# Kernel optimization log

Measured on AMD Instinct MI355X. Metric: run time of the kernel, lower is better.

## Reference

```python
import jax, jax.numpy as jnp
import numpy as np

N, D, H, C, ED, E = 50000, 128, 8, 16, 16, 800000  # nodes, model dim, heads, head dim, edge dim, edges

def _layer_norm(x, g, b, eps=1e-5):
    mu = x.mean(-1, keepdims=True)
    var = ((x - mu) ** 2).mean(-1, keepdims=True)
    return (x - mu) * jax.lax.rsqrt(var + eps) * g + b

def setup_inputs() -> dict:
    key = jax.random.key(0)
    ks = jax.random.split(key, 24)
    s = 0.05
    inp = {
        'x': jax.random.normal(ks[0], (N, D), jnp.float32),
        'edge_index': jax.random.randint(ks[1], (2, E), 0, N, jnp.int32),
        'edge_attr': jax.random.normal(ks[2], (E, ED), jnp.float32),
        # TransformerConv params (Linear convention: y = x @ W + b)
        'wq': s * jax.random.normal(ks[3], (D, H * C)), 'bq': s * jax.random.normal(ks[4], (H * C,)),
        'wk': s * jax.random.normal(ks[5], (D, H * C)), 'bk': s * jax.random.normal(ks[6], (H * C,)),
        'wv': s * jax.random.normal(ks[7], (D, H * C)), 'bv': s * jax.random.normal(ks[8], (H * C,)),
        'we': s * jax.random.normal(ks[9], (ED, H * C)),            # lin_edge, bias=False
        'wskip': s * jax.random.normal(ks[10], (D, H * C)), 'bskip': s * jax.random.normal(ks[11], (H * C,)),
        'wbeta': s * jax.random.normal(ks[12], (3 * H * C, 1)),     # lin_beta, bias=False
        # norms
        'ln1_g': 1.0 + s * jax.random.normal(ks[13], (D,)), 'ln1_b': s * jax.random.normal(ks[14], (D,)),
        'ln2_g': 1.0 + s * jax.random.normal(ks[15], (D,)), 'ln2_b': s * jax.random.normal(ks[16], (D,)),
        # FFN
        'w1': s * jax.random.normal(ks[17], (D, 2 * D)), 'b1': s * jax.random.normal(ks[18], (2 * D,)),
        'w2': s * jax.random.normal(ks[19], (2 * D, D)), 'b2': s * jax.random.normal(ks[20], (D,)),
    }
    return inp

def reference(x, edge_index, edge_attr, wq, bq, wk, bk, wv, bv, we, wskip, bskip, wbeta,
              ln1_g, ln1_b, ln2_g, ln2_b, w1, b1, w2, b2):
    src, dst = edge_index[0], edge_index[1]  # message flows src (j) -> dst (i)
    # --- pre-norm + TransformerConv (beta=True, concat=True, eval-mode dropout=identity) ---
    xn = _layer_norm(x, ln1_g, ln1_b)
    q = (xn @ wq + bq).reshape(N, H, C)
    k = (xn @ wk + bk).reshape(N, H, C)
    v = (xn @ wv + bv).reshape(N, H, C)
    e = (edge_attr @ we).reshape(E, H, C)
    kj = k[src] + e                                     # [E,H,C]
    alpha = (q[dst] * kj).sum(-1) / jnp.sqrt(jnp.float32(C))  # [E,H]
    # segment softmax over incoming edges per destination node
    m = jax.ops.segment_max(alpha, dst, num_segments=N)        # [N,H]
    ea = jnp.exp(alpha - m[dst])
    denom = jax.ops.segment_sum(ea, dst, num_segments=N)
    alpha = ea / (denom[dst] + 1e-16)
    msg = (v[src] + e) * alpha[..., None]               # [E,H,C]
    out = jax.ops.segment_sum(msg, dst, num_segments=N).reshape(N, H * C)
    # beta-gated skip
    x_r = xn @ wskip + bskip
    beta = jax.nn.sigmoid(jnp.concatenate([out, x_r, out - x_r], axis=-1) @ wbeta)  # [N,1]
    out = beta * x_r + (1.0 - beta) * out
    x = x + out
    # --- pre-norm FFN ---
    h = _layer_norm(x, ln2_g, ln2_b)
    h = jax.nn.gelu(h @ w1 + b1, approximate=False) @ w2 + b2
    return x + h
```

## Files before the change

kernel.cpp:

```cpp
#include <hip/hip_runtime.h>
#include <math.h>

#define N_NODES 50000
#define D_MODEL 128
#define N_HEADS 8
#define HEAD_C 16
#define E_DIM 16
#define N_EDGES 800000

typedef __attribute__((ext_vector_type(8))) short bf16x8;
typedef __attribute__((ext_vector_type(4))) float f32x4;

__device__ inline ushort f2bf(float f) {
    unsigned u = __float_as_uint(f);
    unsigned r = (u + 0x7fffu + ((u >> 16) & 1u)) >> 16;
    return (ushort)r;
}
__device__ inline float bf2f(ushort h) { return __uint_as_float(((unsigned)h) << 16); }
__device__ inline uint pack2(float a, float b) {
    return (uint)f2bf(a) | ((uint)f2bf(b) << 16);
}
__device__ inline float gelu_f(float v) {
    return 0.5f * v * (1.0f + erff(v * 0.70710678118654752f));
}

__global__ void prep_weights(const float* __restrict__ wq, const float* __restrict__ wk,
                             const float* __restrict__ wv, const float* __restrict__ wsk,
                             const float* __restrict__ bq, const float* __restrict__ bk,
                             const float* __restrict__ bv, const float* __restrict__ bsk,
                             const float* __restrict__ w1, const float* __restrict__ w2,
                             ushort* __restrict__ wqkvsT, float* __restrict__ bqkvs,
                             ushort* __restrict__ w1T, ushort* __restrict__ w2T,
                             int* __restrict__ deg)
{
    int idx = blockIdx.x * 256 + threadIdx.x;
    {
        int m = idx >> 7, kk = idx & 127;
        int b = m >> 7, ch = m & 127;
        const float* src = (b == 0) ? wq : (b == 1) ? wk : (b == 2) ? wv : wsk;
        wqkvsT[idx] = f2bf(src[kk * 128 + ch]);
    }
    if (idx < 256 * 128) {
        int m = idx >> 7, k = idx & 127;
        w1T[idx] = f2bf(w1[k * 256 + m]);
    }
    if (idx < 128 * 256) {
        int m = idx >> 8, k = idx & 255;
        w2T[idx] = f2bf(w2[k * 128 + m]);
    }
    if (idx < 512) {
        int b = idx >> 7, ch = idx & 127;
        const float* bb = (b == 0) ? bq : (b == 1) ? bk : (b == 2) ? bv : bsk;
        bqkvs[idx] = bb[ch];
    }
    if (idx < N_NODES) deg[idx] = 0;
}

__global__ __launch_bounds__(256) void proj_ln_gemm(
    const float* __restrict__ X, const float* __restrict__ ln_g, const float* __restrict__ ln_b,
    const ushort* __restrict__ WT, const float* __restrict__ bias,
    ushort* __restrict__ Y, int nrows)
{
    __shared__ __align__(16) ushort Al[128 * 128];
    __shared__ __align__(16) ushort Wl[128 * 128];
    int tid = threadIdx.x;
    int wv = tid >> 6, lane = tid & 63;
    int row0 = blockIdx.x * 128;
    int col0 = blockIdx.y * 128;

    int c16 = tid & 15;
    float4 g0 = *(const float4*)&ln_g[c16 * 8];
    float4 g1 = *(const float4*)&ln_g[c16 * 8 + 4];
    float4 bb0 = *(const float4*)&ln_b[c16 * 8];
    float4 bb1 = *(const float4*)&ln_b[c16 * 8 + 4];

    #pragma unroll
    for (int i = 0; i < 8; ++i) {
        int c = tid + i * 256;
        int r = c >> 4;
        int gr = row0 + r;
        float4 xa = make_float4(0.f, 0.f, 0.f, 0.f), xb = xa;
        if (gr < nrows) {
            xa = *(const float4*)&X[(size_t)gr * 128 + c16 * 8];
            xb = *(const float4*)&X[(size_t)gr * 128 + c16 * 8 + 4];
        }
        float s  = xa.x + xa.y + xa.z + xa.w + xb.x + xb.y + xb.z + xb.w;
        float ss = xa.x*xa.x + xa.y*xa.y + xa.z*xa.z + xa.w*xa.w
                 + xb.x*xb.x + xb.y*xb.y + xb.z*xb.z + xb.w*xb.w;
        #pragma unroll
        for (int m = 1; m < 16; m <<= 1) {
            s  += __shfl_xor(s,  m, 64);
            ss += __shfl_xor(ss, m, 64);
        }
        float mu  = s * (1.0f / 128.0f);
        float var = ss * (1.0f / 128.0f) - mu * mu;
        float rs  = rsqrtf(var + 1e-5f);
        ushort h[8];
        h[0] = f2bf((xa.x - mu) * rs * g0.x + bb0.x);
        h[1] = f2bf((xa.y - mu) * rs * g0.y + bb0.y);
        h[2] = f2bf((xa.z - mu) * rs * g0.z + bb0.z);
        h[3] = f2bf((xa.w - mu) * rs * g0.w + bb0.w);
        h[4] = f2bf((xb.x - mu) * rs * g1.x + bb1.x);
        h[5] = f2bf((xb.y - mu) * rs * g1.y + bb1.y);
        h[6] = f2bf((xb.z - mu) * rs * g1.z + bb1.z);
        h[7] = f2bf((xb.w - mu) * rs * g1.w + bb1.w);
        int byte = r * 256 + ((c16 * 16) ^ ((r & 7) << 4));
        *(ulonglong2*)((char*)Al + byte) = *(ulonglong2*)h;
    }
    #pragma unroll
    for (int i = 0; i < 8; ++i) {
        int c = tid + i * 256;
        int r = c >> 4, cc = c & 15;
        ulonglong2 val = *(const ulonglong2*)(WT + (size_t)(col0 + r) * 128 + cc * 8);
        int byte = r * 256 + ((cc * 16) ^ ((r & 7) << 4));
        *(ulonglong2*)((char*)Wl + byte) = val;
    }
    __syncthreads();

    f32x4 acc[2][8];
    #pragma unroll
    for (int i = 0; i < 2; ++i)
        #pragma unroll
        for (int j = 0; j < 8; ++j) acc[i][j] = (f32x4){0.f, 0.f, 0.f, 0.f};
    #pragma unroll
    for (int ks = 0; ks < 4; ++ks) {
        bf16x8 af[2], bfr[8];
        #pragma unroll
        for (int rt = 0; rt < 2; ++rt) {
            int r = wv * 32 + rt * 16 + (lane & 15);
            int byte = r * 256 + ((ks * 64 + (lane >> 4) * 16) ^ ((r & 7) << 4));
            af[rt] = *(const bf16x8*)((const char*)Al + byte);
        }
        #pragma unroll
        for (int ct = 0; ct < 8; ++ct) {
            int r = ct * 16 + (lane & 15);
            int byte = r * 256 + ((ks * 64 + (lane >> 4) * 16) ^ ((r & 7) << 4));
            bfr[ct] = *(const bf16x8*)((const char*)Wl + byte);
        }
        #pragma unroll
        for (int rt = 0; rt < 2; ++rt)
            #pragma unroll
            for (int ct = 0; ct < 8; ++ct)
                acc[rt][ct] = __builtin_amdgcn_mfma_f32_16x16x32_bf16(
                    af[rt], bfr[ct], acc[rt][ct], 0, 0, 0);
    }
    #pragma unroll
    for (int rt = 0; rt < 2; ++rt) {
        #pragma unroll
        for (int ct = 0; ct < 8; ++ct) {
            int gcol = col0 + ct * 16 + (lane & 15);
            float bv = bias[gcol];
            #pragma unroll
            for (int r = 0; r < 4; ++r) {
                int grow = row0 + wv * 32 + rt * 16 + (lane >> 4) * 4 + r;
                if (grow >= nrows) continue;
                Y[(size_t)grow * 512 + gcol] = f2bf(acc[rt][ct][r] + bv);
            }
        }
    }
}

__global__ __launch_bounds__(256) void ffn_fused(
    const ushort* __restrict__ A, const ushort* __restrict__ W1T,
    const ushort* __restrict__ W2T, const float* __restrict__ b1,
    const float* __restrict__ b2, const float* __restrict__ xnew,
    float* __restrict__ out, int nrows)
{
    __shared__ __align__(16) ushort Xl[128 * 128];
    __shared__ __align__(16) ushort W1l[64 * 128];
    __shared__ __align__(16) ushort Hl[128 * 64];
    __shared__ __align__(16) ushort W2l[128 * 64];
    int tid = threadIdx.x;
    int wv = tid >> 6, lane = tid & 63;
    int row0 = blockIdx.x * 128;

    #pragma unroll
    for (int i = 0; i < 8; ++i) {
        int c = tid + i * 256;
        int r = c >> 4, c16 = c & 15;
        int gr = row0 + r;
        ulonglong2 val = {0ull, 0ull};
        if (gr < nrows) val = *(const ulonglong2*)(A + (size_t)gr * 128 + c16 * 8);
        int byte = r * 256 + ((c16 * 16) ^ ((r & 7) << 4));
        *(ulonglong2*)((char*)Xl + byte) = val;
    }

    f32x4 acc2[2][8];
    #pragma unroll
    for (int i = 0; i < 2; ++i)
        #pragma unroll
        for (int j = 0; j < 8; ++j) acc2[i][j] = (f32x4){0.f, 0.f, 0.f, 0.f};

    for (int q = 0; q < 4; ++q) {
        #pragma unroll
        for (int i = 0; i < 4; ++i) {
            int c = tid + i * 256;
            int r = c >> 4, cc = c & 15;
            ulonglong2 val = *(const ulonglong2*)(W1T + (size_t)(q * 64 + r) * 128 + cc * 8);
            int byte = r * 256 + ((cc * 16) ^ ((r & 7) << 4));
            *(ulonglong2*)((char*)W1l + byte) = val;
        }
        #pragma unroll
        for (int i = 0; i < 4; ++i) {
            int c = tid + i * 256;
            int r = c >> 3, c8 = c & 7;
            ulonglong2 val = *(const ulonglong2*)(W2T + (size_t)r * 256 + q * 64 + c8 * 8);
            int byte = r * 128 + ((c8 * 16) ^ ((r & 7) << 4));
            *(ulonglong2*)((char*)W2l + byte) = val;
        }
        __syncthreads();

        f32x4 acc1[2][4];
        #pragma unroll
        for (int i = 0; i < 2; ++i)
            #pragma unroll
            for (int j = 0; j < 4; ++j) acc1[i][j] = (f32x4){0.f, 0.f, 0.f, 0.f};
        #pragma unroll
        for (int ks = 0; ks < 4; ++ks) {
            bf16x8 af[2], bfr[4];
            #pragma unroll
            for (int rt = 0; rt < 2; ++rt) {
                int r = wv * 32 + rt * 16 + (lane & 15);
                int byte = r * 256 + ((ks * 64 + (lane >> 4) * 16) ^ ((r & 7) << 4));
                af[rt] = *(const bf16x8*)((const char*)Xl + byte);
            }
            #pragma unroll
            for (int ct = 0; ct < 4; ++ct) {
                int r = ct * 16 + (lane & 15);
                int byte = r * 256 + ((ks * 64 + (lane >> 4) * 16) ^ ((r & 7) << 4));
                bfr[ct] = *(const bf16x8*)((const char*)W1l + byte);
            }
            #pragma unroll
            for (int rt = 0; rt < 2; ++rt)
                #pragma unroll
                for (int ct = 0; ct < 4; ++ct)
                    acc1[rt][ct] = __builtin_amdgcn_mfma_f32_16x16x32_bf16(
                        af[rt], bfr[ct], acc1[rt][ct], 0, 0, 0);
        }
        #pragma unroll
        for (int rt = 0; rt < 2; ++rt) {
            #pragma unroll
            for (int ct = 0; ct < 4; ++ct) {
                int cl = ct * 16 + (lane & 15);
                float bv = b1[q * 64 + cl];
                #pragma unroll
                for (int r = 0; r < 4; ++r) {
                    int row = wv * 32 + rt * 16 + (lane >> 4) * 4 + r;
                    float v = gelu_f(acc1[rt][ct][r] + bv);
                    int cb = cl * 2;
                    int byte = row * 128 + ((cb & ~15) ^ ((row & 7) << 4)) + (cb & 15);
                    *(ushort*)((char*)Hl + byte) = f2bf(v);
                }
            }
        }
        __syncthreads();

        #pragma unroll
        for (int ks = 0; ks < 2; ++ks) {
            bf16x8 af[2], bfr[8];
            #pragma unroll
            for (int rt = 0; rt < 2; ++rt) {
                int row = wv * 32 + rt * 16 + (lane & 15);
                int byte = row * 128 + ((ks * 64 + (lane >> 4) * 16) ^ ((row & 7) << 4));
                af[rt] = *(const bf16x8*)((const char*)Hl + byte);
            }
            #pragma unroll
            for (int ct = 0; ct < 8; ++ct) {
                int r = ct * 16 + (lane & 15);
                int byte = r * 128 + ((ks * 64 + (lane >> 4) * 16) ^ ((r & 7) << 4));
                bfr[ct] = *(const bf16x8*)((const char*)W2l + byte);
            }
            #pragma unroll
            for (int rt = 0; rt < 2; ++rt)
                #pragma unroll
                for (int ct = 0; ct < 8; ++ct)
                    acc2[rt][ct] = __builtin_amdgcn_mfma_f32_16x16x32_bf16(
                        af[rt], bfr[ct], acc2[rt][ct], 0, 0, 0);
        }
        __syncthreads();
    }

    #pragma unroll
    for (int rt = 0; rt < 2; ++rt) {
        #pragma unroll
        for (int ct = 0; ct < 8; ++ct) {
            int gcol = ct * 16 + (lane & 15);
            float bv = b2[gcol];
            #pragma unroll
            for (int r = 0; r < 4; ++r) {
                int grow = row0 + wv * 32 + rt * 16 + (lane >> 4) * 4 + r;
                if (grow >= nrows) continue;
                size_t idx = (size_t)grow * 128 + gcol;
                out[idx] = acc2[rt][ct][r] + bv + xnew[idx];
            }
        }
    }
}

__global__ void hist_kernel(const int* __restrict__ dst, int* __restrict__ deg)
{
    int e = blockIdx.x * 256 + threadIdx.x;
    if (e < N_EDGES) atomicAdd(&deg[dst[e]], 1);
}

__global__ void scan1_kernel(const int* __restrict__ deg, int* __restrict__ off,
                             int* __restrict__ bsum)
{
    __shared__ int sm[256];
    int i = blockIdx.x * 256 + threadIdx.x;
    int v = (i < N_NODES) ? deg[i] : 0;
    sm[threadIdx.x] = v;
    __syncthreads();
    #pragma unroll
    for (int d = 1; d < 256; d <<= 1) {
        int t = (threadIdx.x >= d) ? sm[threadIdx.x - d] : 0;
        __syncthreads();
        sm[threadIdx.x] += t;
        __syncthreads();
    }
    if (i < N_NODES) off[i] = sm[threadIdx.x] - v;
    if (threadIdx.x == 255) bsum[blockIdx.x] = sm[255];
}

__global__ void scan2_kernel(int* __restrict__ bsum, int nb)
{
    __shared__ int sm[256];
    int v = (threadIdx.x < nb) ? bsum[threadIdx.x] : 0;
    sm[threadIdx.x] = v;
    __syncthreads();
    #pragma unroll
    for (int d = 1; d < 256; d <<= 1) {
        int t = (threadIdx.x >= d) ? sm[threadIdx.x - d] : 0;
        __syncthreads();
        sm[threadIdx.x] += t;
        __syncthreads();
    }
    if (threadIdx.x < nb) bsum[threadIdx.x] = sm[threadIdx.x] - v;
}

__global__ void scan3_kernel(int* __restrict__ off, const int* __restrict__ bsum,
                             int* __restrict__ cursor)
{
    int i = blockIdx.x * 256 + threadIdx.x;
    if (i < N_NODES) {
        int o = off[i] + bsum[blockIdx.x];
        off[i] = o;
        cursor[i] = o;
    }
}

__global__ void scatter_kernel(const int* __restrict__ dst, const int* __restrict__ src,
                               const float* __restrict__ eattr, int* __restrict__ cursor,
                               int* __restrict__ src_s, ushort* __restrict__ eattr_s)
{
    int e = blockIdx.x * 256 + threadIdx.x;
    if (e < N_EDGES) {
        int p = atomicAdd(&cursor[dst[e]], 1);
        src_s[p] = src[e];
        const float4* s4 = (const float4*)(eattr + (size_t)e * E_DIM);
        float4 f0 = s4[0], f1 = s4[1], f2 = s4[2], f3 = s4[3];
        uint4 u0, u1;
        u0.x = pack2(f0.x, f0.y); u0.y = pack2(f0.z, f0.w);
        u0.z = pack2(f1.x, f1.y); u0.w = pack2(f1.z, f1.w);
        u1.x = pack2(f2.x, f2.y); u1.y = pack2(f2.z, f2.w);
        u1.z = pack2(f3.x, f3.y); u1.w = pack2(f3.z, f3.w);
        uint4* d4 = (uint4*)(eattr_s + (size_t)p * E_DIM);
        d4[0] = u0; d4[1] = u1;
    }
}

#define ATTN_STEP(P, S, A0, A1, E0, E1) do {                                         \
    int sv_ = src_s[P];                                                              \
    uint eap_ = *(const uint*)(eattr_s + (size_t)(P) * E_DIM + j2);                  \
    float ea0_ = bf2f((ushort)eap_), ea1_ = bf2f((ushort)(eap_ >> 16));              \
    size_t sb_ = (size_t)sv_ * 512;                                                  \
    uint kp_ = *(const uint*)(qkvs + sb_ + 128 + 2 * lane);                          \
    uint vp_ = *(const uint*)(qkvs + sb_ + 256 + 2 * lane);                          \
    float p_ = q0 * bf2f((ushort)kp_) + q1 * bf2f((ushort)(kp_ >> 16))               \
             + ea0_ * qp0 + ea1_ * qp1;                                              \
    p_ += __shfl_xor(p_, 1, 64);                                                     \
    p_ += __shfl_xor(p_, 2, 64);                                                     \
    p_ += __shfl_xor(p_, 4, 64);                                                     \
    float w_ = __expf(fminf(p_, 60.f));                                              \
    S  += w_;                                                                        \
    A0 += w_ * bf2f((ushort)vp_);                                                    \
    A1 += w_ * bf2f((ushort)(vp_ >> 16));                                            \
    E0 += w_ * ea0_;                                                                 \
    E1 += w_ * ea1_;                                                                 \
} while (0)

__global__ void node_attn(const ushort* __restrict__ qkvs, const float* __restrict__ x,
                          const float* __restrict__ we, const float* __restrict__ wbeta,
                          const float* __restrict__ ln2g, const float* __restrict__ ln2b,
                          const int* __restrict__ off, const int* __restrict__ deg,
                          const int* __restrict__ src_s, const ushort* __restrict__ eattr_s,
                          float* __restrict__ xnew, ushort* __restrict__ h2)
{
    __shared__ float wl[E_DIM * 128];
    __shared__ float weT[128 * 17];
    __shared__ float sc4[4][128];
    for (int t = threadIdx.x; t < E_DIM * 32; t += 256)
        *(float4*)&wl[t * 4] = *(const float4*)&we[t * 4];
    for (int t = threadIdx.x; t < E_DIM * 128; t += 256) {
        int j = t >> 7, ch = t & 127;
        weT[ch * 17 + j] = we[t];
    }
    __syncthreads();

    int nl   = threadIdx.x >> 6;
    int node = blockIdx.x * 4 + nl;
    int lane = threadIdx.x & 63;
    if (node >= N_NODES) return;

    int j2 = (lane & 7) * 2;
    int hb = (lane >> 3) * 16;

    size_t nb = (size_t)node * 512;
    uint qp = *(const uint*)(qkvs + nb + 2 * lane);
    float q0r = bf2f((ushort)qp), q1r = bf2f((ushort)(qp >> 16));

    sc4[nl][2 * lane]     = q0r;
    sc4[nl][2 * lane + 1] = q1r;
    float qp0 = 0.f, qp1 = 0.f;
    #pragma unroll
    for (int c = 0; c < 16; ++c) {
        float qc = sc4[nl][hb + c];
        qp0 += qc * weT[(hb + c) * 17 + j2];
        qp1 += qc * weT[(hb + c) * 17 + j2 + 1];
    }
    float q0 = q0r * 0.25f, q1 = q1r * 0.25f;
    qp0 *= 0.25f; qp1 *= 0.25f;

    float SA = 0.f, A0a = 0.f, A1a = 0.f, E0a = 0.f, E1a = 0.f;
    float SB = 0.f, A0b = 0.f, A1b = 0.f, E0b = 0.f, E1b = 0.f;

    int o = off[node], dg = deg[node];
    int i = 0;
    for (; i + 2 <= dg; i += 2) {
        ATTN_STEP(o + i,     SA, A0a, A1a, E0a, E1a);
        ATTN_STEP(o + i + 1, SB, A0b, A1b, E0b, E1b);
    }
    if (i < dg)
        ATTN_STEP(o + i, SA, A0a, A1a, E0a, E1a);

    float S  = SA + SB;
    float A0 = A0a + A0b, A1 = A1a + A1b;
    float E0 = E0a + E0b, E1 = E1a + E1b;

    sc4[nl][2 * lane]     = E0;
    sc4[nl][2 * lane + 1] = E1;
    float ep0 = 0.f, ep1 = 0.f;
    #pragma unroll
    for (int j = 0; j < 16; ++j) {
        float es = sc4[nl][hb + j];
        ep0 += es * wl[j * 128 + 2 * lane];
        ep1 += es * wl[j * 128 + 2 * lane + 1];
    }

    float rinv = 1.f / (S + 1e-16f);
    float o0 = (A0 + ep0) * rinv;
    float o1 = (A1 + ep1) * rinv;

    uint xrp = *(const uint*)(qkvs + nb + 384 + 2 * lane);
    float xr0 = bf2f((ushort)xrp), xr1 = bf2f((ushort)(xrp >> 16));
    float2 wb0 = *(const float2*)&wbeta[2 * lane];
    float2 wb1 = *(const float2*)&wbeta[128 + 2 * lane];
    float2 wb2 = *(const float2*)&wbeta[256 + 2 * lane];
    float dot = o0 * wb0.x + o1 * wb0.y + xr0 * wb1.x + xr1 * wb1.y
              + (o0 - xr0) * wb2.x + (o1 - xr1) * wb2.y;
    #pragma unroll
    for (int w = 32; w > 0; w >>= 1) dot += __shfl_xor(dot, w, 64);
    float beta = 1.f / (1.f + __expf(-dot));

    size_t xb = (size_t)node * D_MODEL + 2 * lane;
    float2 xv = *(const float2*)&x[xb];
    float ox = xv.x + beta * xr0 + (1.f - beta) * o0;
    float oy = xv.y + beta * xr1 + (1.f - beta) * o1;
    *(float2*)&xnew[xb] = make_float2(ox, oy);

    float s2  = ox + oy;
    float ss2 = ox * ox + oy * oy;
    #pragma unroll
    for (int w = 32; w > 0; w >>= 1) {
        s2  += __shfl_xor(s2,  w, 64);
        ss2 += __shfl_xor(ss2, w, 64);
    }
    float mu  = s2 * (1.0f / 128.0f);
    float var = ss2 * (1.0f / 128.0f) - mu * mu;
    float rs  = rsqrtf(var + 1e-5f);
    float2 g2 = *(const float2*)&ln2g[2 * lane];
    float2 b2 = *(const float2*)&ln2b[2 * lane];
    float h0 = (ox - mu) * rs * g2.x + b2.x;
    float h1 = (oy - mu) * rs * g2.y + b2.y;
    ((uint*)h2)[(size_t)node * 64 + lane] = pack2(h0, h1);
}

extern "C" void kernel_launch(void* const* d_in, const int* in_sizes, int n_in,
                              void* d_out, int out_size, void* d_ws, size_t ws_size,
                              hipStream_t stream)
{
    const float* x     = (const float*)d_in[0];
    const int*   eidx  = (const int*)  d_in[1];
    const float* eattr = (const float*)d_in[2];
    const float* wq  = (const float*)d_in[3];  const float* bq  = (const float*)d_in[4];
    const float* wk  = (const float*)d_in[5];  const float* bk  = (const float*)d_in[6];
    const float* wv  = (const float*)d_in[7];  const float* bv  = (const float*)d_in[8];
    const float* we  = (const float*)d_in[9];
    const float* wsk = (const float*)d_in[10]; const float* bsk = (const float*)d_in[11];
    const float* wbeta = (const float*)d_in[12];
    const float* ln1g = (const float*)d_in[13]; const float* ln1b = (const float*)d_in[14];
    const float* ln2g = (const float*)d_in[15]; const float* ln2b = (const float*)d_in[16];
    const float* w1 = (const float*)d_in[17]; const float* b1 = (const float*)d_in[18];
    const float* w2 = (const float*)d_in[19]; const float* b2 = (const float*)d_in[20];
    const int* srcp = eidx;
    const int* dstp = eidx + N_EDGES;
    float* out = (float*)d_out;

    char* w = (char*)d_ws;
    size_t o = 0;
    ushort* qkvs_b  = (ushort*)(w + o);  o += (size_t)N_NODES * 512 * 2;
    float* xnew = (float*)(w + o);  o += (size_t)N_NODES * 128 * 4;
    ushort* eattr_s = (ushort*)(w + o); o += (size_t)N_EDGES * E_DIM * 2;
    int* src_s = (int*)(w + o);     o += (size_t)N_EDGES * 4;
    ushort* h2_b = (ushort*)(w + o); o += (size_t)N_NODES * 128 * 2;
    ushort* wqkvsT = (ushort*)(w + o); o += 512 * 128 * 2;
    ushort* w1T    = (ushort*)(w + o); o += 256 * 128 * 2;
    ushort* w2T    = (ushort*)(w + o); o += 128 * 256 * 2;
    float*  bqkvs  = (float*)(w + o);  o += 4096;
    int* deg    = (int*)(w + o); o += 200704;
    int* offb   = (int*)(w + o); o += 200704;
    int* cursor = (int*)(w + o); o += 200704;
    int* bsum   = (int*)(w + o); o += 4096;

    dim3 blk(256);
    dim3 lngrid((N_NODES + 3) / 4);
    const int NB = (N_NODES + 255) / 256;
    const int EB = (N_EDGES + 255) / 256;
    const int GB = (N_NODES + 127) / 128;

    prep_weights<<<dim3(256), blk, 0, stream>>>(wq, wk, wv, wsk, bq, bk, bv, bsk,
                                                w1, w2, wqkvsT, bqkvs, w1T, w2T, deg);
    proj_ln_gemm<<<dim3(GB, 4), blk, 0, stream>>>(x, ln1g, ln1b, wqkvsT, bqkvs,
                                                  qkvs_b, N_NODES);
    hist_kernel<<<dim3(EB), blk, 0, stream>>>(dstp, deg);
    scan1_kernel<<<dim3(NB), blk, 0, stream>>>(deg, offb, bsum);
    scan2_kernel<<<dim3(1), blk, 0, stream>>>(bsum, NB);
    scan3_kernel<<<dim3(NB), blk, 0, stream>>>(offb, bsum, cursor);
    scatter_kernel<<<dim3(EB), blk, 0, stream>>>(dstp, srcp, eattr, cursor, src_s, eattr_s);
    node_attn<<<lngrid, blk, 0, stream>>>(qkvs_b, x, we, wbeta, ln2g, ln2b,
                                          offb, deg, src_s, eattr_s, xnew, h2_b);
    ffn_fused<<<dim3(GB), blk, 0, stream>>>(h2_b, w1T, w2T, b1, b2, xnew, out, N_NODES);
}
```

Before: 293.9 us.

## Interleave K/V into packed per-node buffer and fuse CSR scan into one kernel

Adds a repack kernel that interleaves each node's K and V bf16 pairs into one 8-byte element per lane, so the edge gather in node_attn issues one 64-bit load instead of two separate 32-bit loads from distant offsets. The three-kernel block scan is replaced by a single 1024-thread block that does a chunked sequential scan, removing two launches. This costs an extra pass over K/V and a serial single-block scan whose per-thread chunk reads are strided and uncoalesced.

```diff
diff --git a/kernel.cpp b/kernel.cpp
--- a/kernel.cpp
+++ b/kernel.cpp
@@ -160,6 +160,17 @@
     }
 }
 
+__global__ void repack_kv(const ushort* __restrict__ qkvs, uint2* __restrict__ kv16)
+{
+    int idx = blockIdx.x * 256 + threadIdx.x;
+    if (idx >= N_NODES * 64) return;
+    int node = idx >> 6, u = idx & 63;
+    size_t nb = (size_t)node * 512;
+    uint kp = *(const uint*)(qkvs + nb + 128 + 2 * u);
+    uint vp = *(const uint*)(qkvs + nb + 256 + 2 * u);
+    kv16[idx] = make_uint2(kp, vp);
+}
+
 __global__ __launch_bounds__(256) void ffn_fused(
     const ushort* __restrict__ A, const ushort* __restrict__ W1T,
     const ushort* __restrict__ W2T, const float* __restrict__ b1,
@@ -303,49 +314,35 @@
     if (e < N_EDGES) atomicAdd(&deg[dst[e]], 1);
 }
 
-__global__ void scan1_kernel(const int* __restrict__ deg, int* __restrict__ off,
-                             int* __restrict__ bsum)
-{
-    __shared__ int sm[256];
-    int i = blockIdx.x * 256 + threadIdx.x;
-    int v = (i < N_NODES) ? deg[i] : 0;
-    sm[threadIdx.x] = v;
+__global__ __launch_bounds__(1024) void scan_fused(const int* __restrict__ deg,
+                                                   int* __restrict__ off,
+                                                   int* __restrict__ cursor)
+{
+    __shared__ int part[1024];
+    const int CH = (N_NODES + 1023) / 1024;
+    int t = threadIdx.x;
+    int base = t * CH;
+    int sum = 0;
+    for (int i = 0; i < CH; ++i) {
+        int idx = base + i;
+        if (idx < N_NODES) sum += deg[idx];
+    }
+    part[t] = sum;
     __syncthreads();
-    #pragma unroll
-    for (int d = 1; d < 256; d <<= 1) {
-        int t = (threadIdx.x >= d) ? sm[threadIdx.x - d] : 0;
+    for (int d = 1; d < 1024; d <<= 1) {
+        int v = (t >= d) ? part[t - d] : 0;
         __syncthreads();
-        sm[threadIdx.x] += t;
+        part[t] += v;
         __syncthreads();
     }
-    if (i < N_NODES) off[i] = sm[threadIdx.x] - v;
-    if (threadIdx.x == 255) bsum[blockIdx.x] = sm[255];
-}
-
-__global__ void scan2_kernel(int* __restrict__ bsum, int nb)
-{
-    __shared__ int sm[256];
-    int v = (threadIdx.x < nb) ? bsum[threadIdx.x] : 0;
-    sm[threadIdx.x] = v;
-    __syncthreads();
-    #pragma unroll
-    for (int d = 1; d < 256; d <<= 1) {
-        int t = (threadIdx.x >= d) ? sm[threadIdx.x - d] : 0;
-        __syncthreads();
-        sm[threadIdx.x] += t;
-        __syncthreads();
-    }
-    if (threadIdx.x < nb) bsum[threadIdx.x] = sm[threadIdx.x] - v;
-}
-
-__global__ void scan3_kernel(int* __restrict__ off, const int* __restrict__ bsum,
-                             int* __restrict__ cursor)
-{
-    int i = blockIdx.x * 256 + threadIdx.x;
-    if (i < N_NODES) {
-        int o = off[i] + bsum[blockIdx.x];
-        off[i] = o;
-        cursor[i] = o;
+    int run = (t > 0) ? part[t - 1] : 0;
+    for (int i = 0; i < CH; ++i) {
+        int idx = base + i;
+        if (idx < N_NODES) {
+            off[idx] = run;
+            cursor[idx] = run;
+            run += deg[idx];
+        }
     }
 }
 
@@ -373,23 +370,22 @@
     int sv_ = src_s[P];                                                              \
     uint eap_ = *(const uint*)(eattr_s + (size_t)(P) * E_DIM + j2);                  \
     float ea0_ = bf2f((ushort)eap_), ea1_ = bf2f((ushort)(eap_ >> 16));              \
-    size_t sb_ = (size_t)sv_ * 512;                                                  \
-    uint kp_ = *(const uint*)(qkvs + sb_ + 128 + 2 * lane);                          \
-    uint vp_ = *(const uint*)(qkvs + sb_ + 256 + 2 * lane);                          \
-    float p_ = q0 * bf2f((ushort)kp_) + q1 * bf2f((ushort)(kp_ >> 16))               \
+    uint2 kv_ = kv16[(size_t)sv_ * 64 + lane];                                       \
+    float p_ = q0 * bf2f((ushort)kv_.x) + q1 * bf2f((ushort)(kv_.x >> 16))           \
              + ea0_ * qp0 + ea1_ * qp1;                                              \
     p_ += __shfl_xor(p_, 1, 64);                                                     \
     p_ += __shfl_xor(p_, 2, 64);                                                     \
     p_ += __shfl_xor(p_, 4, 64);                                                     \
     float w_ = __expf(fminf(p_, 60.f));                                              \
     S  += w_;                                                                        \
-    A0 += w_ * bf2f((ushort)vp_);                                                    \
-    A1 += w_ * bf2f((ushort)(vp_ >> 16));                                            \
+    A0 += w_ * bf2f((ushort)kv_.y);                                                  \
+    A1 += w_ * bf2f((ushort)(kv_.y >> 16));                                          \
     E0 += w_ * ea0_;                                                                 \
     E1 += w_ * ea1_;                                                                 \
 } while (0)
 
-__global__ void node_attn(const ushort* __restrict__ qkvs, const float* __restrict__ x,
+__global__ void node_attn(const ushort* __restrict__ qkvs, const uint2* __restrict__ kv16,
+                          const float* __restrict__ x,
                           const float* __restrict__ we, const float* __restrict__ wbeta,
                           const float* __restrict__ ln2g, const float* __restrict__ ln2b,
                           const int* __restrict__ off, const int* __restrict__ deg,
@@ -523,6 +519,7 @@
     ushort* eattr_s = (ushort*)(w + o); o += (size_t)N_EDGES * E_DIM * 2;
     int* src_s = (int*)(w + o);     o += (size_t)N_EDGES * 4;
     ushort* h2_b = (ushort*)(w + o); o += (size_t)N_NODES * 128 * 2;
+    uint2* kv16 = (uint2*)(w + o);  o += (size_t)N_NODES * 64 * 8;
     ushort* wqkvsT = (ushort*)(w + o); o += 512 * 128 * 2;
     ushort* w1T    = (ushort*)(w + o); o += 256 * 128 * 2;
     ushort* w2T    = (ushort*)(w + o); o += 128 * 256 * 2;
@@ -530,11 +527,9 @@
     int* deg    = (int*)(w + o); o += 200704;
     int* offb   = (int*)(w + o); o += 200704;
     int* cursor = (int*)(w + o); o += 200704;
-    int* bsum   = (int*)(w + o); o += 4096;
 
     dim3 blk(256);
     dim3 lngrid((N_NODES + 3) / 4);
-    const int NB = (N_NODES + 255) / 256;
     const int EB = (N_EDGES + 255) / 256;
     const int GB = (N_NODES + 127) / 128;
 
@@ -542,12 +537,11 @@
                                                 w1, w2, wqkvsT, bqkvs, w1T, w2T, deg);
     proj_ln_gemm<<<dim3(GB, 4), blk, 0, stream>>>(x, ln1g, ln1b, wqkvsT, bqkvs,
                                                   qkvs_b, N_NODES);
+    repack_kv<<<dim3((N_NODES * 64 + 255) / 256), blk, 0, stream>>>(qkvs_b, kv16);
     hist_kernel<<<dim3(EB), blk, 0, stream>>>(dstp, deg);
-    scan1_kernel<<<dim3(NB), blk, 0, stream>>>(deg, offb, bsum);
-    scan2_kernel<<<dim3(1), blk, 0, stream>>>(bsum, NB);
-    scan3_kernel<<<dim3(NB), blk, 0, stream>>>(offb, bsum, cursor);
+    scan_fused<<<dim3(1), dim3(1024), 0, stream>>>(deg, offb, cursor);
     scatter_kernel<<<dim3(EB), blk, 0, stream>>>(dstp, srcp, eattr, cursor, src_s, eattr_s);
-    node_attn<<<lngrid, blk, 0, stream>>>(qkvs_b, x, we, wbeta, ln2g, ln2b,
+    node_attn<<<lngrid, blk, 0, stream>>>(qkvs_b, kv16, x, we, wbeta, ln2g, ln2b,
                                           offb, deg, src_s, eattr_s, xnew, h2_b);
     ffn_fused<<<dim3(GB), blk, 0, stream>>>(h2_b, w1T, w2T, b1, b2, xnew, out, N_NODES);
 }
```

New measurement: 426.9 us. +45.3%, slower.
